# Kernel optimization log

Hardware: AMD Instinct MI355X
Metric: run time of the kernel (lower is better)

The kernel has to match this reference:

```python
import jax, jax.numpy as jnp
import numpy as np

N = 1024
NFEAT = 512
H1, H2, NCLASS = 128, 64, 64
ALPHA = 0.2
NEG = -9e15  # torch uses -9000000000000000.0


def setup_inputs() -> dict:
    key = jax.random.key(0)
    ks = jax.random.split(key, 20)
    nrm = lambda k, shape, s=0.05: jax.random.normal(k, shape, jnp.float32) * s
    x = jax.random.normal(ks[0], (N, NFEAT), jnp.float32)
    adj = jax.random.randint(ks[1], (N, N), 0, 2, jnp.int32)
    W1 = nrm(ks[2], (NFEAT, H1)); a1 = nrm(ks[3], (2 * H1,)); b1 = nrm(ks[4], (H1,))
    W2 = nrm(ks[5], (H1, H2));    a2 = nrm(ks[6], (2 * H2,)); b2 = nrm(ks[7], (H2,))
    W3 = nrm(ks[8], (H2, NCLASS)); a3 = nrm(ks[9], (2 * NCLASS,)); b3 = nrm(ks[10], (NCLASS,))
    D = N * NCLASS  # 64 * args.edge with edge == N
    l1w = nrm(ks[11], (6, 256, D)); l1b = nrm(ks[12], (6, 256))
    l2w = nrm(ks[13], (6, 128, 256)); l2b = nrm(ks[14], (6, 128))
    l3w = nrm(ks[15], (6, 1, 128)); l3b = nrm(ks[16], (6, 1))
    return dict(x=x, adj=adj, W1=W1, a1=a1, b1=b1, W2=W2, a2=a2, b2=b2,
                W3=W3, a3=a3, b3=b3, l1w=l1w, l1b=l1b, l2w=l2w, l2b=l2b,
                l3w=l3w, l3b=l3b)


def gat_layer(x, mask, W, a, b):
    h = x @ W                                  # [N, F]
    n, f = h.shape
    # torch: a_input = cat([h.repeat(N,1).view(N*N,-1), h.repeat(1,N).view(-1,N*N).T], 1)
    # first half at pair (i,j) is h[j]  ->  contributes (h @ a[:f])[j]
    e1 = h @ a[:f]                             # [N]
    # second half is the (scrambled) view: tile(h,(1,N)).reshape(f, n*n), dotted with a[f:]
    T = jnp.tile(h, (1, n)).reshape(f, n * n)  # faithful to the torch view semantics
    e2 = (a[f:] @ T).reshape(n, n)             # [N, N]
    e = jax.nn.leaky_relu(e1[None, :] + e2, ALPHA)
    e = jnp.where(mask, e, NEG)
    att = jax.nn.softmax(e, axis=1)            # dropout omitted (eval mode)
    return jax.nn.relu(att @ h) + b


def reference(x, adj, W1, a1, b1, W2, a2, b2, W3, a3, b3,
              l1w, l1b, l2w, l2b, l3w, l3b):
    mask = adj > 0
    h = jax.nn.relu(gat_layer(x, mask, W1, a1, b1))
    h = jax.nn.relu(gat_layer(h, mask, W2, a2, b2))
    h = jax.nn.relu(gat_layer(h, mask, W3, a3, b3))
    xf = h.reshape(-1)                         # [N * NCLASS]
    t = jax.nn.relu(jnp.einsum('hok,k->ho', l1w, xf) + l1b)      # [6, 256]
    t = jax.nn.sigmoid(jnp.einsum('hot,ht->ho', l2w, t) + l2b)   # [6, 128]
    out = jnp.einsum('hot,ht->ho', l3w, t) + l3b                 # [6, 1]
    return out
```

## Files before the change

kernel.cpp:

```cpp
#include <hip/hip_runtime.h>
#include <hip/hip_bf16.h>

#define NROW 1024

typedef float f4v __attribute__((ext_vector_type(4)));

__device__ __forceinline__ float wave_reduce(float v) {
    for (int off = 32; off; off >>= 1) v += __shfl_down(v, off);
    return v;
}

template <int K, int F>
__global__ void __launch_bounds__(1024) gemm_e1_kernel(const float* __restrict__ in,
                                                       const float* __restrict__ W,
                                                       const float* __restrict__ a,
                                                       float* __restrict__ h,
                                                       float* __restrict__ e1) {
    __shared__ float srow[4 * K];
    __shared__ float pacc[1024];
    __shared__ float redf[8];
    int t = threadIdx.x;
    int i0 = blockIdx.x * 4;
    for (int idx = t; idx < 4 * K; idx += 1024) srow[idx] = in[i0 * K + idx];
    __syncthreads();
    {
        int c = t & (F - 1);
        int rh = t / F;
        int r = rh & 3, half = rh >> 2;
        const float* sp = srow + r * K + half * (K / 2);
        const float* wp = W + (size_t)(half * (K / 2)) * F + c;
        float a0 = 0.f, a1 = 0.f;
#pragma unroll 4
        for (int k = 0; k < K / 2; k += 2) {
            a0 = fmaf(sp[k], wp[(size_t)k * F], a0);
            a1 = fmaf(sp[k + 1], wp[(size_t)(k + 1) * F], a1);
        }
        pacc[t] = a0 + a1;
    }
    __syncthreads();
    if (t < 4 * F) {
        float accf = pacc[t] + pacc[t + 4 * F];
        int c = t & (F - 1), r = t / F;
        h[(i0 + r) * F + c] = accf;
        float p = wave_reduce(accf * a[c]);
        if ((t & 63) == 0) redf[t >> 6] = p;
    }
    __syncthreads();
    constexpr int WPR = F / 64;
    if (t < 4) {
        float s = 0.f;
#pragma unroll
        for (int w = 0; w < WPR; ++w) s += redf[t * WPR + w];
        e1[i0 + t] = s;
    }
}

template <int F, int G>
__device__ __forceinline__ void attn_core(const float* __restrict__ h,
                                          const int* __restrict__ adj,
                                          const float* __restrict__ e1in,
                                          const float* __restrict__ aprev,
                                          const float* __restrict__ bprev, int i0,
                                          float* wexp_sh, float* E2row, float* cred,
                                          float* redf, float* sinv,
                                          unsigned long long* msk, float* orow) {
    constexpr int NQ = 1024 / F;
    int t = threadIdx.x;
    int ib = i0 / F;
    {
        int g = t / F, c = t % F;
        float acc = 0.f;
#pragma unroll 4
        for (int p = g; p < F; p += NQ) acc = fmaf(aprev[F + p], h[(p * G + ib) * F + c], acc);
        cred[t] = acc;
    }
    __syncthreads();
    if (t < F) {
        float s = 0.f;
#pragma unroll
        for (int g = 0; g < NQ; ++g) s += cred[g * F + t];
        E2row[t] = s;
    }
    __syncthreads();
    if (t < NROW) {
        float v = e1in[t] + E2row[t & (F - 1)];
        v = v > 0.f ? v : 0.2f * v;
        wexp_sh[t] = expf(v);
    }
    __syncthreads();
    int lane = t & 63, wv = t >> 6;
    {
        int r = wv & 3;
        const int* arow = adj + (size_t)(i0 + r) * NROW;
        float s = 0.f;
        for (int jb = (wv >> 2); jb < 16; jb += 4) {
            int j = jb * 64 + lane;
            bool on = arow[j] > 0;
            unsigned long long m = __ballot(on);
            if (lane == 0) msk[r * 16 + jb] = m;
            s += on ? wexp_sh[j] : 0.f;
        }
        s = wave_reduce(s);
        if (lane == 0) redf[wv] = s;
    }
    __syncthreads();
    if (t < 4) sinv[t] = 1.f / (redf[t] + redf[t + 4] + redf[t + 8] + redf[t + 12]);
    __syncthreads();
    int c = t % F, q = t / F;
    float acc0 = 0.f, acc1 = 0.f, acc2 = 0.f, acc3 = 0.f;
    const unsigned long long* m0 = msk;
    const unsigned long long* m1 = msk + 16;
    const unsigned long long* m2 = msk + 32;
    const unsigned long long* m3 = msk + 48;
    for (int jb = 0; jb < 16; ++jb) {
        unsigned long long k0 = m0[jb] >> q, k1 = m1[jb] >> q,
                           k2 = m2[jb] >> q, k3 = m3[jb] >> q;
#pragma unroll
        for (int ss = 0; ss < 64 / NQ; ++ss) {
            int j = jb * 64 + q + ss * NQ;
            float w = wexp_sh[j];
            float hv = h[j * F + c];
            acc0 = fmaf((k0 & 1) ? w : 0.f, hv, acc0);
            acc1 = fmaf((k1 & 1) ? w : 0.f, hv, acc1);
            acc2 = fmaf((k2 & 1) ? w : 0.f, hv, acc2);
            acc3 = fmaf((k3 & 1) ? w : 0.f, hv, acc3);
            k0 >>= NQ; k1 >>= NQ; k2 >>= NQ; k3 >>= NQ;
        }
    }
    float* cr = cred + t * 4;
    cr[0] = acc0; cr[1] = acc1; cr[2] = acc2; cr[3] = acc3;
    __syncthreads();
    if (t < 4 * F) {
        int rr = t / F, cc = t % F;
        float tot = 0.f;
#pragma unroll
        for (int qq = 0; qq < NQ; ++qq) tot += cred[(qq * F + cc) * 4 + rr];
        float v = tot * sinv[rr];
        v = v > 0.f ? v : 0.f;
        v += bprev[cc];
        v = v > 0.f ? v : 0.f;
        orow[rr * F + cc] = v;
    }
    __syncthreads();
}

template <int F, int G, int FN>
__global__ void __launch_bounds__(1024) attn_gemm_kernel(
    const float* __restrict__ h, const int* __restrict__ adj,
    const float* __restrict__ e1in, const float* __restrict__ aprev,
    const float* __restrict__ bprev, const float* __restrict__ Wn,
    const float* __restrict__ an, float* __restrict__ hout,
    float* __restrict__ e1out) {
    __shared__ float wexp_sh[1024];
    __shared__ float E2row[F];
    __shared__ float cred[4096];
    __shared__ float redf[16];
    __shared__ float sinv[4];
    __shared__ float orow[4 * F];
    __shared__ unsigned long long msk[64];
    int i0 = blockIdx.x * 4;
    attn_core<F, G>(h, adj, e1in, aprev, bprev, i0, wexp_sh, E2row, cred, redf, sinv, msk, orow);
    int t = threadIdx.x;
    if (t < 4 * FN) {
        int r = t / FN, c = t % FN;
        float acc = 0.f;
#pragma unroll 8
        for (int k = 0; k < F; ++k) acc = fmaf(orow[r * F + k], Wn[k * FN + c], acc);
        hout[(i0 + r) * FN + c] = acc;
        float p = wave_reduce(acc * an[c]);
        if ((t & 63) == 0) redf[r] = p;
    }
    __syncthreads();
    if (t < 4) e1out[i0 + t] = redf[t];
}

template <int F, int G>
__global__ void __launch_bounds__(1024) attn_xf_kernel(
    const float* __restrict__ h, const int* __restrict__ adj,
    const float* __restrict__ e1in, const float* __restrict__ aprev,
    const float* __restrict__ bprev, float* __restrict__ xf) {
    __shared__ float wexp_sh[1024];
    __shared__ float E2row[F];
    __shared__ float cred[4096];
    __shared__ float redf[16];
    __shared__ float sinv[4];
    __shared__ float orow[4 * F];
    __shared__ unsigned long long msk[64];
    int i0 = blockIdx.x * 4;
    attn_core<F, G>(h, adj, e1in, aprev, bprev, i0, wexp_sh, E2row, cred, redf, sinv, msk, orow);
    int t = threadIdx.x;
    if (t < 4 * F) xf[(size_t)i0 * F + t] = orow[t];
}

__global__ void __launch_bounds__(512) head1_kernel(const float* __restrict__ l1w,
                                                    const float* __restrict__ l1b,
                                                    const float* __restrict__ xf,
                                                    float* __restrict__ t1g) {
    __shared__ float red[16];
    int t = threadIdx.x;
    int r0 = blockIdx.x * 2;
    const f4v* xv = (const f4v*)xf;
    const f4v* w0p = (const f4v*)l1w + (size_t)r0 * 16384;
    const f4v* w1p = w0p + 16384;
    float a0a = 0.f, a0b = 0.f, a1a = 0.f, a1b = 0.f;
#pragma unroll 4
    for (int it = t; it < 16384; it += 512) {
        f4v xx = xv[it];
        f4v w0 = __builtin_nontemporal_load(&w0p[it]);
        f4v w1 = __builtin_nontemporal_load(&w1p[it]);
        a0a = fmaf(w0.x, xx.x, fmaf(w0.y, xx.y, a0a));
        a0b = fmaf(w0.z, xx.z, fmaf(w0.w, xx.w, a0b));
        a1a = fmaf(w1.x, xx.x, fmaf(w1.y, xx.y, a1a));
        a1b = fmaf(w1.z, xx.z, fmaf(w1.w, xx.w, a1b));
    }
    float acc0 = wave_reduce(a0a + a0b);
    float acc1 = wave_reduce(a1a + a1b);
    int lane = t & 63, wv = t >> 6;
    if (lane == 0) { red[wv * 2] = acc0; red[wv * 2 + 1] = acc1; }
    __syncthreads();
    if (t < 2) {
        int row = r0 + t;
        float s = l1b[row];
#pragma unroll
        for (int w = 0; w < 8; ++w) s += red[w * 2 + t];
        t1g[row] = s > 0.f ? s : 0.f;
    }
}

__global__ void __launch_bounds__(256) head23_kernel(
    const float* __restrict__ t1g, const float* __restrict__ l2w,
    const float* __restrict__ l2b, const float* __restrict__ l3w,
    const float* __restrict__ l3b, float* __restrict__ out) {
    __shared__ float t1s[256];
    __shared__ float t2s[128];
    int hh = blockIdx.x, t = threadIdx.x, lane = t & 63, wv = t >> 6;
    t1s[t] = t1g[hh * 256 + t];
    __syncthreads();
    float4 tv = ((const float4*)t1s)[lane];
    for (int o = wv; o < 128; o += 4) {
        float4 w4 = ((const float4*)(l2w + ((size_t)hh * 128 + o) * 256))[lane];
        float p = fmaf(w4.x, tv.x, fmaf(w4.y, tv.y, fmaf(w4.z, tv.z, w4.w * tv.w)));
        p = wave_reduce(p);
        if (lane == 0) t2s[o] = 1.f / (1.f + expf(-(p + l2b[hh * 128 + o])));
    }
    __syncthreads();
    if (wv == 0) {
        float p = l3w[hh * 128 + lane] * t2s[lane] +
                  l3w[hh * 128 + 64 + lane] * t2s[64 + lane];
        p = wave_reduce(p);
        if (lane == 0) out[hh] = p + l3b[hh];
    }
}

extern "C" void kernel_launch(void* const* d_in, const int* in_sizes, int n_in,
                              void* d_out, int out_size, void* d_ws, size_t ws_size,
                              hipStream_t stream) {
    const float* x   = (const float*)d_in[0];
    const int*   adj = (const int*)d_in[1];
    const float* W1  = (const float*)d_in[2];
    const float* a1  = (const float*)d_in[3];
    const float* b1  = (const float*)d_in[4];
    const float* W2  = (const float*)d_in[5];
    const float* a2  = (const float*)d_in[6];
    const float* b2  = (const float*)d_in[7];
    const float* W3  = (const float*)d_in[8];
    const float* a3  = (const float*)d_in[9];
    const float* b3  = (const float*)d_in[10];
    const float* l1w = (const float*)d_in[11];
    const float* l1b = (const float*)d_in[12];
    const float* l2w = (const float*)d_in[13];
    const float* l2b = (const float*)d_in[14];
    const float* l3w = (const float*)d_in[15];
    const float* l3b = (const float*)d_in[16];
    float* out = (float*)d_out;

    float* ws = (float*)d_ws;
    float* h1   = ws;
    float* h2   = ws + 131072;
    float* h3   = ws + 196608;
    float* xf   = ws + 262144;
    float* e1a  = ws + 327680;
    float* e1b  = ws + 328704;
    float* e1c  = ws + 329728;
    float* t1g  = ws + 330752;

    gemm_e1_kernel<512, 128><<<256, 1024, 0, stream>>>(x, W1, a1, h1, e1a);
    attn_gemm_kernel<128, 8, 64><<<256, 1024, 0, stream>>>(h1, adj, e1a, a1, b1, W2, a2, h2, e1b);
    attn_gemm_kernel<64, 16, 64><<<256, 1024, 0, stream>>>(h2, adj, e1b, a2, b2, W3, a3, h3, e1c);
    attn_xf_kernel<64, 16><<<256, 1024, 0, stream>>>(h3, adj, e1c, a3, b3, xf);
    head1_kernel<<<768, 512, 0, stream>>>(l1w, l1b, xf, t1g);
    head23_kernel<<<6, 256, 0, stream>>>(t1g, l2w, l2b, l3w, l3b, out);
}
```

Before: 153.2 us.

## Precompute masked attention weights in LDS and fuse head layers via last-block counter

```diff
diff --git a/kernel.cpp b/kernel.cpp
--- a/kernel.cpp
+++ b/kernel.cpp
@@ -15,11 +15,13 @@
                                                        const float* __restrict__ W,
                                                        const float* __restrict__ a,
                                                        float* __restrict__ h,
-                                                       float* __restrict__ e1) {
+                                                       float* __restrict__ e1,
+                                                       unsigned* __restrict__ cnt) {
     __shared__ float srow[4 * K];
     __shared__ float pacc[1024];
     __shared__ float redf[8];
     int t = threadIdx.x;
+    if (blockIdx.x == 0 && t == 0) *cnt = 0u;
     int i0 = blockIdx.x * 4;
     for (int idx = t; idx < 4 * K; idx += 1024) srow[idx] = in[i0 * K + idx];
     __syncthreads();
@@ -63,7 +65,7 @@
                                           const float* __restrict__ bprev, int i0,
                                           float* wexp_sh, float* E2row, float* cred,
                                           float* redf, float* sinv,
-                                          unsigned long long* msk, float* orow) {
+                                          f4v* alpha4, float* orow) {
     constexpr int NQ = 1024 / F;
     int t = threadIdx.x;
     int ib = i0 / F;
@@ -82,7 +84,7 @@
         E2row[t] = s;
     }
     __syncthreads();
-    if (t < NROW) {
+    {
         float v = e1in[t] + E2row[t & (F - 1)];
         v = v > 0.f ? v : 0.2f * v;
         wexp_sh[t] = expf(v);
@@ -93,12 +95,12 @@
         int r = wv & 3;
         const int* arow = adj + (size_t)(i0 + r) * NROW;
         float s = 0.f;
+        float* al = (float*)alpha4;
         for (int jb = (wv >> 2); jb < 16; jb += 4) {
             int j = jb * 64 + lane;
-            bool on = arow[j] > 0;
-            unsigned long long m = __ballot(on);
-            if (lane == 0) msk[r * 16 + jb] = m;
-            s += on ? wexp_sh[j] : 0.f;
+            float av = (arow[j] > 0) ? wexp_sh[j] : 0.f;
+            al[j * 4 + r] = av;
+            s += av;
         }
         s = wave_reduce(s);
         if (lane == 0) redf[wv] = s;
@@ -108,24 +110,14 @@
     __syncthreads();
     int c = t % F, q = t / F;
     float acc0 = 0.f, acc1 = 0.f, acc2 = 0.f, acc3 = 0.f;
-    const unsigned long long* m0 = msk;
-    const unsigned long long* m1 = msk + 16;
-    const unsigned long long* m2 = msk + 32;
-    const unsigned long long* m3 = msk + 48;
-    for (int jb = 0; jb < 16; ++jb) {
-        unsigned long long k0 = m0[jb] >> q, k1 = m1[jb] >> q,
-                           k2 = m2[jb] >> q, k3 = m3[jb] >> q;
-#pragma unroll
-        for (int ss = 0; ss < 64 / NQ; ++ss) {
-            int j = jb * 64 + q + ss * NQ;
-            float w = wexp_sh[j];
-            float hv = h[j * F + c];
-            acc0 = fmaf((k0 & 1) ? w : 0.f, hv, acc0);
-            acc1 = fmaf((k1 & 1) ? w : 0.f, hv, acc1);
-            acc2 = fmaf((k2 & 1) ? w : 0.f, hv, acc2);
-            acc3 = fmaf((k3 & 1) ? w : 0.f, hv, acc3);
-            k0 >>= NQ; k1 >>= NQ; k2 >>= NQ; k3 >>= NQ;
-        }
+#pragma unroll 8
+    for (int j = q; j < NROW; j += NQ) {
+        f4v al = alpha4[j];
+        float hv = h[j * F + c];
+        acc0 = fmaf(al.x, hv, acc0);
+        acc1 = fmaf(al.y, hv, acc1);
+        acc2 = fmaf(al.z, hv, acc2);
+        acc3 = fmaf(al.w, hv, acc3);
     }
     float* cr = cred + t * 4;
     cr[0] = acc0; cr[1] = acc1; cr[2] = acc2; cr[3] = acc3;
@@ -157,9 +149,9 @@
     __shared__ float redf[16];
     __shared__ float sinv[4];
     __shared__ float orow[4 * F];
-    __shared__ unsigned long long msk[64];
+    __shared__ f4v alpha4[1024];
     int i0 = blockIdx.x * 4;
-    attn_core<F, G>(h, adj, e1in, aprev, bprev, i0, wexp_sh, E2row, cred, redf, sinv, msk, orow);
+    attn_core<F, G>(h, adj, e1in, aprev, bprev, i0, wexp_sh, E2row, cred, redf, sinv, alpha4, orow);
     int t = threadIdx.x;
     if (t < 4 * FN) {
         int r = t / FN, c = t % FN;
@@ -185,18 +177,23 @@
     __shared__ float redf[16];
     __shared__ float sinv[4];
     __shared__ float orow[4 * F];
-    __shared__ unsigned long long msk[64];
+    __shared__ f4v alpha4[1024];
     int i0 = blockIdx.x * 4;
-    attn_core<F, G>(h, adj, e1in, aprev, bprev, i0, wexp_sh, E2row, cred, redf, sinv, msk, orow);
+    attn_core<F, G>(h, adj, e1in, aprev, bprev, i0, wexp_sh, E2row, cred, redf, sinv, alpha4, orow);
     int t = threadIdx.x;
     if (t < 4 * F) xf[(size_t)i0 * F + t] = orow[t];
 }
 
-__global__ void __launch_bounds__(512) head1_kernel(const float* __restrict__ l1w,
-                                                    const float* __restrict__ l1b,
-                                                    const float* __restrict__ xf,
-                                                    float* __restrict__ t1g) {
+__global__ void __launch_bounds__(512) head1_kernel(
+    const float* __restrict__ l1w, const float* __restrict__ l1b,
+    const float* __restrict__ xf, float* __restrict__ t1g,
+    const float* __restrict__ l2w, const float* __restrict__ l2b,
+    const float* __restrict__ l3w, const float* __restrict__ l3b,
+    float* __restrict__ out, unsigned* __restrict__ cnt) {
     __shared__ float red[16];
+    __shared__ float t1s[1536];
+    __shared__ float t2s[768];
+    __shared__ int isLast;
     int t = threadIdx.x;
     int r0 = blockIdx.x * 2;
     const f4v* xv = (const f4v*)xf;
@@ -225,30 +222,27 @@
         for (int w = 0; w < 8; ++w) s += red[w * 2 + t];
         t1g[row] = s > 0.f ? s : 0.f;
     }
-}
-
-__global__ void __launch_bounds__(256) head23_kernel(
-    const float* __restrict__ t1g, const float* __restrict__ l2w,
-    const float* __restrict__ l2b, const float* __restrict__ l3w,
-    const float* __restrict__ l3b, float* __restrict__ out) {
-    __shared__ float t1s[256];
-    __shared__ float t2s[128];
-    int hh = blockIdx.x, t = threadIdx.x, lane = t & 63, wv = t >> 6;
-    t1s[t] = t1g[hh * 256 + t];
-    __syncthreads();
-    float4 tv = ((const float4*)t1s)[lane];
-    for (int o = wv; o < 128; o += 4) {
-        float4 w4 = ((const float4*)(l2w + ((size_t)hh * 128 + o) * 256))[lane];
+    __threadfence();
+    __syncthreads();
+    if (t == 0) isLast = (atomicAdd(cnt, 1u) == 767u) ? 1 : 0;
+    __syncthreads();
+    if (!isLast) return;
+    __threadfence();
+    for (int i = t; i < 1536; i += 512) t1s[i] = t1g[i];
+    __syncthreads();
+    for (int o = wv; o < 768; o += 8) {
+        float4 w4 = ((const float4*)(l2w + (size_t)o * 256))[lane];
+        float4 tv = ((const float4*)(t1s + (o >> 7) * 256))[lane];
         float p = fmaf(w4.x, tv.x, fmaf(w4.y, tv.y, fmaf(w4.z, tv.z, w4.w * tv.w)));
         p = wave_reduce(p);
-        if (lane == 0) t2s[o] = 1.f / (1.f + expf(-(p + l2b[hh * 128 + o])));
-    }
-    __syncthreads();
-    if (wv == 0) {
-        float p = l3w[hh * 128 + lane] * t2s[lane] +
-                  l3w[hh * 128 + 64 + lane] * t2s[64 + lane];
+        if (lane == 0) t2s[o] = 1.f / (1.f + expf(-(p + l2b[o])));
+    }
+    __syncthreads();
+    if (wv < 6) {
+        float p = l3w[wv * 128 + lane] * t2s[wv * 128 + lane] +
+                  l3w[wv * 128 + 64 + lane] * t2s[wv * 128 + 64 + lane];
         p = wave_reduce(p);
-        if (lane == 0) out[hh] = p + l3b[hh];
+        if (lane == 0) out[wv] = p + l3b[wv];
     }
 }
 
@@ -283,11 +277,11 @@
     float* e1b  = ws + 328704;
     float* e1c  = ws + 329728;
     float* t1g  = ws + 330752;
-
-    gemm_e1_kernel<512, 128><<<256, 1024, 0, stream>>>(x, W1, a1, h1, e1a);
+    unsigned* cnt = (unsigned*)(ws + 332288);
+
+    gemm_e1_kernel<512, 128><<<256, 1024, 0, stream>>>(x, W1, a1, h1, e1a, cnt);
     attn_gemm_kernel<128, 8, 64><<<256, 1024, 0, stream>>>(h1, adj, e1a, a1, b1, W2, a2, h2, e1b);
     attn_gemm_kernel<64, 16, 64><<<256, 1024, 0, stream>>>(h2, adj, e1b, a2, b2, W3, a3, h3, e1c);
     attn_xf_kernel<64, 16><<<256, 1024, 0, stream>>>(h3, adj, e1c, a3, b3, xf);
-    head1_kernel<<<768, 512, 0, stream>>>(l1w, l1b, xf, t1g);
-    head23_kernel<<<6, 256, 0, stream>>>(t1g, l2w, l2b, l3w, l3b, out);
-}
+    head1_kernel<<<768, 512, 0, stream>>>(l1w, l1b, xf, t1g, l2w, l2b, l3w, l3b, out, cnt);
+}
```

Measured after the change: 408.1 us. 166% more time.
